# Optimization experiments

Hardware: AMD Instinct MI355X
Metric: run time of the kernel (lower is better)

The kernel has to match this reference:

```python
import jax, jax.numpy as jnp
from jax import lax
import numpy as np

D_MODEL, N_STATES, N_GROUPS, K_CONV = 1024, 16, 8, 4
BATCH, LENGTH = 2, 2048


def setup_inputs() -> dict:
    key = jax.random.key(0)
    ks = jax.random.split(key, 8)
    x = jax.random.normal(ks[0], (BATCH, LENGTH, D_MODEL), dtype=jnp.float32)
    in_proj_w = jax.random.normal(ks[1], (2 * D_MODEL, D_MODEL), dtype=jnp.float32) * 0.02
    in_proj_b = jnp.zeros((2 * D_MODEL,), dtype=jnp.float32)
    delta_proj_w = jax.random.uniform(ks[2], (D_MODEL, D_MODEL), dtype=jnp.float32, minval=0.001, maxval=0.1)
    a_log = jnp.log(jnp.tile(jnp.arange(1, N_STATES + 1, dtype=jnp.float32), (D_MODEL, 1)))
    b_proj_w = jax.random.normal(ks[3], (N_GROUPS * N_STATES, D_MODEL), dtype=jnp.float32) * 1e-4
    b_proj_b = jnp.zeros((N_GROUPS * N_STATES,), dtype=jnp.float32)
    c_param = jax.random.normal(ks[4], (D_MODEL, N_STATES), dtype=jnp.float32) * 0.02
    # depthwise conv (groups = d_model): kernel [D, 1, K]
    conv_w = jax.random.normal(ks[5], (D_MODEL, 1, K_CONV), dtype=jnp.float32) * (1.0 / np.sqrt(K_CONV))
    conv_b = jnp.zeros((D_MODEL,), dtype=jnp.float32)
    return {"x": x, "in_proj_w": in_proj_w, "in_proj_b": in_proj_b,
            "delta_proj_w": delta_proj_w, "a_log": a_log,
            "b_proj_w": b_proj_w, "b_proj_b": b_proj_b, "c_param": c_param,
            "conv_w": conv_w, "conv_b": conv_b}


def _causal_conv(u, conv_w, conv_b):
    # u: [B, L, D] -> depthwise causal conv along L
    D = u.shape[-1]
    K = conv_w.shape[-1]
    uc = jnp.transpose(u, (0, 2, 1))  # [B, D, L]
    uc = lax.conv_general_dilated(uc, conv_w, window_strides=(1,),
                                  padding=[(K - 1, 0)], feature_group_count=D,
                                  dimension_numbers=("NCH", "OIH", "NCH"))
    uc = uc + conv_b[None, :, None]
    return jnp.transpose(uc, (0, 2, 1))  # [B, L, D]


def _selective_scan(delta, A, Bmat, c_param, u):
    # delta,u: [B,L,D]; A: [D,N]; Bmat: [B,L,G,N]; c_param: [D,N]
    Bsz, L, D = delta.shape
    N = A.shape[1]
    G = Bmat.shape[2]
    Bexp = jnp.repeat(Bmat, D // G, axis=2)            # [B,L,D,N]
    dA = jnp.exp(delta[..., None] * A)                  # [B,L,D,N]
    dBu = (delta * u)[..., None] * Bexp                 # [B,L,D,N]

    def step(h, xs):
        da, dbu = xs
        h = da * h + dbu                                # [B,D,N]
        y = jnp.einsum("bdn,dn->bd", h, c_param)
        return h, y

    h0 = jnp.zeros((Bsz, D, N), dtype=delta.dtype)
    _, ys = lax.scan(step, h0, (jnp.moveaxis(dA, 1, 0), jnp.moveaxis(dBu, 1, 0)))
    return jnp.moveaxis(ys, 0, 1)                       # [B,L,D]


def reference(x, in_proj_w, in_proj_b, delta_proj_w, a_log, b_proj_w, b_proj_b, c_param, conv_w, conv_b):
    Bsz, L, _ = x.shape
    N = a_log.shape[1]
    G = b_proj_w.shape[0] // N
    xp = x @ in_proj_w.T + in_proj_b                    # [B,L,2D]
    u, v = jnp.split(xp, 2, axis=-1)
    delta = jax.nn.softplus(u @ delta_proj_w.T)         # [B,L,D]
    A = -jnp.exp(a_log)                                 # [D,N]
    Bmat = (u @ b_proj_w.T + b_proj_b).reshape(Bsz, L, G, N)
    u_conv = jax.nn.silu(_causal_conv(u, conv_w, conv_b))
    y = _selective_scan(delta, A, Bmat, c_param, u_conv)
    return y * jax.nn.silu(v)
```

## Files before the change

### kernel.cpp

```cpp
#include <hip/hip_runtime.h>
#include <math.h>

#define LTOT 2048
#define MROWS 4096
#define CHK 64
#define NCH (LTOT / CHK)
#define SPAD 20

typedef short bf16x8 __attribute__((ext_vector_type(8)));
typedef float f32x4  __attribute__((ext_vector_type(4)));

__device__ __forceinline__ unsigned short bf16_rne(float f) {
  unsigned u = __float_as_uint(f);
  u += 0x7FFF + ((u >> 16) & 1);
  return (unsigned short)(u >> 16);
}
__device__ __forceinline__ float bf16_to_f(unsigned short h) {
  return __uint_as_float(((unsigned)h) << 16);
}
__device__ __forceinline__ float softplus_f(float x) {
  return (x > 15.f) ? x : log1pf(expf(x));
}
__device__ __forceinline__ float silu_f(float x) {
  return x / (1.f + expf(-x));
}

__global__ __launch_bounds__(256) void k_prep(
    const float* __restrict__ x, const float* __restrict__ w1,
    const float* __restrict__ dw, const float* __restrict__ bw,
    const float* __restrict__ b1, const float* __restrict__ bb,
    unsigned short* __restrict__ xh, unsigned short* __restrict__ wfh,
    unsigned short* __restrict__ wdbAh, unsigned short* __restrict__ wdbAl,
    unsigned short* __restrict__ w1th, unsigned short* __restrict__ w1tl,
    float* __restrict__ bfull) {
  __shared__ float ts[64][65];
  const int blk = blockIdx.x;
  const int t = threadIdx.x;

  if (blk < 6144) {
    const float* src; unsigned short* h; int i;
    if (blk < 4096) { src = x;  h = xh;  i = blk * 256 + t; }
    else            { src = w1; h = wfh; i = (blk - 4096) * 256 + t; }
    const float4 v = ((const float4*)src)[i];
    ushort4 hh;
    hh.x = bf16_rne(v.x); hh.y = bf16_rne(v.y);
    hh.z = bf16_rne(v.z); hh.w = bf16_rne(v.w);
    ((ushort4*)h)[i] = hh;
  } else if (blk < 7296) {
    const float* src; unsigned short *h, *l; int i;
    if (blk < 7168) { src = dw; h = wdbAh; l = wdbAl; i = (blk - 6144) * 256 + t; }
    else            { src = bw; h = wdbAh + (size_t)1024*1024; l = wdbAl + (size_t)1024*1024;
                      i = (blk - 7168) * 256 + t; }
    const float4 v = ((const float4*)src)[i];
    ushort4 hh, ll;
    hh.x = bf16_rne(v.x); ll.x = bf16_rne(v.x - bf16_to_f(hh.x));
    hh.y = bf16_rne(v.y); ll.y = bf16_rne(v.y - bf16_to_f(hh.y));
    hh.z = bf16_rne(v.z); ll.z = bf16_rne(v.z - bf16_to_f(hh.z));
    hh.w = bf16_rne(v.w); ll.w = bf16_rne(v.w - bf16_to_f(hh.w));
    ((ushort4*)h)[i] = hh;
    ((ushort4*)l)[i] = ll;
  } else if (blk < 7552) {
    const int s = blk - 7296;
    const int k0 = (s & 15) * 64, j0 = (s >> 4) * 64;
    const int r = t >> 4, c4 = (t & 15) * 4;
    #pragma unroll
    for (int p = 0; p < 4; ++p) {
      const int row = p * 16 + r;
      const float4 v = *(const float4*)&w1[(size_t)(j0 + row) * 1024 + k0 + c4];
      ts[row][c4] = v.x; ts[row][c4+1] = v.y; ts[row][c4+2] = v.z; ts[row][c4+3] = v.w;
    }
    __syncthreads();
    #pragma unroll
    for (int p = 0; p < 4; ++p) {
      const int rk = p * 16 + r;
      ushort4 hh, ll;
      float f;
      f = ts[c4+0][rk]; hh.x = bf16_rne(f); ll.x = bf16_rne(f - bf16_to_f(hh.x));
      f = ts[c4+1][rk]; hh.y = bf16_rne(f); ll.y = bf16_rne(f - bf16_to_f(hh.y));
      f = ts[c4+2][rk]; hh.z = bf16_rne(f); ll.z = bf16_rne(f - bf16_to_f(hh.z));
      f = ts[c4+3][rk]; hh.w = bf16_rne(f); ll.w = bf16_rne(f - bf16_to_f(hh.w));
      *(ushort4*)&w1th[(size_t)(k0 + rk) * 1024 + j0 + c4] = hh;
      *(ushort4*)&w1tl[(size_t)(k0 + rk) * 1024 + j0 + c4] = ll;
    }
  } else {
    const int j = (blk - 7552) * 16 + (t >> 4);
    const int lane16 = t & 15;
    const float* W = (j < 1024) ? (dw + (size_t)j * 1024) : (bw + (size_t)(j - 1024) * 1024);
    float s = 0.f;
    for (int i = 0; i < 64; ++i) {
      const int k = lane16 + i * 16;
      s = fmaf(b1[k], W[k], s);
    }
    s += __shfl_xor(s, 8, 16);
    s += __shfl_xor(s, 4, 16);
    s += __shfl_xor(s, 2, 16);
    s += __shfl_xor(s, 1, 16);
    if (lane16 == 0) bfull[j] = s + ((j >= 1024) ? bb[j - 1024] : 0.f);
  }
}

__global__ __launch_bounds__(256) void k_wcomp3(
    const unsigned short* __restrict__ Ah_g, const unsigned short* __restrict__ Al_g,
    const unsigned short* __restrict__ Bh_g, const unsigned short* __restrict__ Bl_g,
    float* __restrict__ part) {
  __shared__ __align__(16) unsigned short LAh[128*32];
  __shared__ __align__(16) unsigned short LAl[128*32];
  __shared__ __align__(16) unsigned short LBh[128*32];
  __shared__ __align__(16) unsigned short LBl[128*32];
  const int t = threadIdx.x;
  const int wave = t >> 6, lane = t & 63;
  const int m0 = blockIdx.y * 128;
  const int n0 = blockIdx.x * 128;
  const int kb = blockIdx.z * 256;
  const int wr = wave >> 1, wc = wave & 1;
  const int ln = lane & 15, kq = lane >> 4;
  const int srow = lane >> 2, scol = (lane & 3) * 8;

  f32x4 acc[4][4];
  #pragma unroll
  for (int i = 0; i < 4; ++i)
    #pragma unroll
    for (int j = 0; j < 4; ++j) acc[i][j] = (f32x4){0.f, 0.f, 0.f, 0.f};

  const unsigned short* pAh = Ah_g + (size_t)m0 * 1024;
  const unsigned short* pAl = Al_g + (size_t)m0 * 1024;
  const unsigned short* pBh = Bh_g + (size_t)n0 * 1024;
  const unsigned short* pBl = Bl_g + (size_t)n0 * 1024;

  auto stage = [&](const unsigned short* g, unsigned short* lds, int k0) {
    #pragma unroll
    for (int r = 0; r < 2; ++r) {
      const unsigned short* gp = g + (size_t)(r * 64 + wave * 16 + srow) * 1024 + k0 + scol;
      unsigned short* lp = lds + (r * 64 + wave * 16) * 32;
      __builtin_amdgcn_global_load_lds((const __attribute__((address_space(1))) void*)gp,
                                       (__attribute__((address_space(3))) void*)lp, 16, 0, 0);
    }
  };

  for (int k0 = kb; k0 < kb + 256; k0 += 32) {
    __syncthreads();
    stage(pAh, LAh, k0);
    stage(pAl, LAl, k0);
    stage(pBh, LBh, k0);
    stage(pBl, LBl, k0);
    __syncthreads();
    bf16x8 ah[4], al[4], bh[4], bl[4];
    #pragma unroll
    for (int i = 0; i < 4; ++i) {
      const int ar = (wr * 64 + i * 16 + ln) * 32 + kq * 8;
      const int br = (wc * 64 + i * 16 + ln) * 32 + kq * 8;
      ah[i] = *(const bf16x8*)&LAh[ar];
      al[i] = *(const bf16x8*)&LAl[ar];
      bh[i] = *(const bf16x8*)&LBh[br];
      bl[i] = *(const bf16x8*)&LBl[br];
    }
    #pragma unroll
    for (int i = 0; i < 4; ++i)
      #pragma unroll
      for (int j = 0; j < 4; ++j) {
        acc[i][j] = __builtin_amdgcn_mfma_f32_16x16x32_bf16(ah[i], bh[j], acc[i][j], 0, 0, 0);
        acc[i][j] = __builtin_amdgcn_mfma_f32_16x16x32_bf16(ah[i], bl[j], acc[i][j], 0, 0, 0);
        acc[i][j] = __builtin_amdgcn_mfma_f32_16x16x32_bf16(al[i], bh[j], acc[i][j], 0, 0, 0);
      }
  }

  float* pout = part + (size_t)blockIdx.z * 1152 * 1024;
  #pragma unroll
  for (int nj = 0; nj < 4; ++nj) {
    const int kcol = n0 + wc * 64 + nj * 16 + ln;
    #pragma unroll
    for (int mi = 0; mi < 4; ++mi) {
      const int i = m0 + wr * 64 + mi * 16 + kq * 4;
      #pragma unroll
      for (int j = 0; j < 4; ++j)
        pout[(size_t)(i + j) * 1024 + kcol] = acc[mi][nj][j];
    }
  }
}

__global__ void k_wred(const float* __restrict__ part, unsigned short* __restrict__ outh) {
  const int e = blockIdx.x * 256 + threadIdx.x;
  const int i = e >> 8;
  const int k4 = (e & 255) * 4;
  const size_t stride = (size_t)1152 * 1024;
  const size_t off = (size_t)i * 1024 + k4;
  float4 s = *(const float4*)&part[off];
  #pragma unroll
  for (int p = 1; p < 4; ++p) {
    const float4 q = *(const float4*)&part[p * stride + off];
    s.x += q.x; s.y += q.y; s.z += q.z; s.w += q.w;
  }
  const int rbase = (i < 1024) ? (2176 + i) : (1024 + i);
  ushort4 hh;
  hh.x = bf16_rne(s.x); hh.y = bf16_rne(s.y); hh.z = bf16_rne(s.z); hh.w = bf16_rne(s.w);
  *(ushort4*)&outh[(size_t)rbase * 1024 + k4] = hh;
}

__global__ __launch_bounds__(256) void k_mm_u(
    const unsigned short* __restrict__ xh, const unsigned short* __restrict__ wfh,
    const float* __restrict__ b1, const float* __restrict__ bfull,
    float* __restrict__ u_, float* __restrict__ v_,
    float* __restrict__ delta, float* __restrict__ Bm) {
  __shared__ __align__(16) unsigned short LA[2][128*64];
  __shared__ __align__(16) unsigned short LB[2][128*64];
  const int t = threadIdx.x;
  const int wave = t >> 6, lane = t & 63;
  const int flat = blockIdx.x;
  const int wg = (flat & 7) * 100 + (flat >> 3);
  const int tn = wg % 25;
  const int m0 = (wg / 25) * 128;
  const int wr = wave >> 1, wc = wave & 1;
  const int ln = lane & 15, kq = lane >> 4;
  const int srow = lane >> 3;
  const int scb  = ((lane & 7) ^ (lane >> 3)) * 8;

  f32x4 acc[4][4];
  #pragma unroll
  for (int i = 0; i < 4; ++i)
    #pragma unroll
    for (int j = 0; j < 4; ++j) acc[i][j] = (f32x4){0.f, 0.f, 0.f, 0.f};

  const unsigned short* pAh = xh + (size_t)m0 * 1024;
  const unsigned short* pBh = wfh + (size_t)(tn * 128) * 1024;

  auto stage = [&](const unsigned short* g, unsigned short* lds, int k0) {
    #pragma unroll
    for (int r = 0; r < 4; ++r) {
      const int rowb = wave * 32 + r * 8;
      const unsigned short* gp = g + (size_t)(rowb + srow) * 1024 + k0 + scb;
      unsigned short* lp = lds + rowb * 64;
      __builtin_amdgcn_global_load_lds((const __attribute__((address_space(1))) void*)gp,
                                       (__attribute__((address_space(3))) void*)lp, 16, 0, 0);
    }
  };

  stage(pAh, LA[0], 0);
  stage(pBh, LB[0], 0);

  for (int tt = 0; tt < 16; ++tt) {
    const int cur = tt & 1;
    if (tt < 15) {
      stage(pAh, LA[cur ^ 1], (tt + 1) * 64);
      stage(pBh, LB[cur ^ 1], (tt + 1) * 64);
      asm volatile("s_waitcnt vmcnt(8)" ::: "memory");
    } else {
      asm volatile("s_waitcnt vmcnt(0)" ::: "memory");
    }
    __builtin_amdgcn_s_barrier();
    __builtin_amdgcn_sched_barrier(0);

    const unsigned short* la = LA[cur];
    const unsigned short* lb = LB[cur];
    #pragma unroll
    for (int kh = 0; kh < 2; ++kh) {
      bf16x8 ah[4], bh[4];
      #pragma unroll
      for (int i = 0; i < 4; ++i) {
        const int arow = wr * 64 + i * 16 + ln;
        const int brow = wc * 64 + i * 16 + ln;
        const int ablk = ((kh * 4 + kq) ^ (arow & 7)) * 8;
        const int bblk = ((kh * 4 + kq) ^ (brow & 7)) * 8;
        ah[i] = *(const bf16x8*)&la[arow * 64 + ablk];
        bh[i] = *(const bf16x8*)&lb[brow * 64 + bblk];
      }
      #pragma unroll
      for (int i = 0; i < 4; ++i)
        #pragma unroll
        for (int j = 0; j < 4; ++j)
          acc[i][j] = __builtin_amdgcn_mfma_f32_16x16x32_bf16(ah[i], bh[j], acc[i][j], 0, 0, 0);
    }

    if (tt < 15) {
      __builtin_amdgcn_sched_barrier(0);
      __builtin_amdgcn_s_barrier();
    }
  }

  #pragma unroll
  for (int nj = 0; nj < 4; ++nj) {
    const int colg = tn * 128 + wc * 64 + nj * 16 + ln;
    float bv;
    if (colg < 2048)      bv = b1[colg];
    else if (colg < 2176) bv = bfull[1024 + colg - 2048];
    else                  bv = bfull[colg - 2176];
    #pragma unroll
    for (int mi = 0; mi < 4; ++mi) {
      const int row = m0 + wr * 64 + mi * 16 + kq * 4;
      #pragma unroll
      for (int j = 0; j < 4; ++j) {
        const float val = acc[mi][nj][j] + bv;
        if (tn < 8)        u_[(size_t)(row + j) * 1024 + colg] = val;
        else if (tn < 16)  v_[(size_t)(row + j) * 1024 + colg - 1024] = val;
        else if (tn == 16) Bm[(size_t)(row + j) * 128 + colg - 2048] = val;
        else               delta[(size_t)(row + j) * 1024 + colg - 2176] = softplus_f(val);
      }
    }
  }
}

__global__ __launch_bounds__(256) void k_scanA(
    const float* __restrict__ delta, const float* __restrict__ u_,
    const float* __restrict__ Bm, const float* __restrict__ a_log,
    const float* __restrict__ cw, const float* __restrict__ cb,
    float* __restrict__ hend, float* __restrict__ Pp)
{
  __shared__ float sru[68][SPAD];
  __shared__ float sd[CHK][SPAD];
  __shared__ float sb[CHK][SPAD];
  __shared__ float suc[CHK][SPAD];
  const int t = threadIdx.x;
  const int bid = blockIdx.x;
  const int dblk = bid & 63;
  const int ch   = (bid >> 6) & (NCH - 1);
  const int b    = bid >> 11;
  const int d0 = dblk * 16;
  const int g  = dblk >> 3;
  const int l0 = ch * CHK;
  const size_t mb = (size_t)b * LTOT;

  {
    const int lrow = t >> 2;
    const int lc4  = (t & 3) * 4;
    const size_t r = mb + l0 + lrow;
    float4 rd = *(const float4*)&delta[r*1024 + d0 + lc4];
    float4 rb = *(const float4*)&Bm[r*128 + g*16 + lc4];
    *(float4*)&sd[lrow][lc4] = rd;
    *(float4*)&sb[lrow][lc4] = rb;
    const int sl = l0 + lrow - 4;
    float4 ru = (sl >= 0) ? *(const float4*)&u_[(mb + sl)*1024 + d0 + lc4]
                          : (float4){0.f, 0.f, 0.f, 0.f};
    *(float4*)&sru[lrow][lc4] = ru;
    if (t < 16) {
      const int rr2 = 64 + (t >> 2);
      const int sl2 = l0 + rr2 - 4;
      float4 r2 = *(const float4*)&u_[(mb + sl2)*1024 + d0 + (t & 3) * 4];
      *(float4*)&sru[rr2][(t & 3) * 4] = r2;
    }
  }
  __syncthreads();
  {
    const int c = t & 15;
    const int rb4 = (t >> 4) * 4;
    const float4 cwf = *(const float4*)&cw[(d0 + c) * 4];
    const float cbf = cb[d0 + c];
    #pragma unroll
    for (int q = 0; q < 4; ++q) {
      const int l = rb4 + q;
      float a = cbf;
      a = fmaf(sru[l+1][c], cwf.x, a);
      a = fmaf(sru[l+2][c], cwf.y, a);
      a = fmaf(sru[l+3][c], cwf.z, a);
      a = fmaf(sru[l+4][c], cwf.w, a);
      suc[l][c] = silu_f(a);
    }
  }
  __syncthreads();

  const int gi = t >> 4;
  const int n  = t & 15;
  const int d  = d0 + gi;
  const float A2 = -expf(a_log[d*16 + n]) * 1.4426950408889634f;

  float h = 0.f, P = 1.f;
  #pragma unroll 8
  for (int l = 0; l < CHK; ++l) {
    const float dv = sd[l][gi];
    const float uv = suc[l][gi];
    const float bv = sb[l][n];
    const float da = exp2f(dv * A2);
    P *= da;
    h = fmaf(da, h, dv * uv * bv);
  }
  const size_t idx = ((size_t)(b*NCH + ch) * 1024 + d) * 16 + n;
  hend[idx] = h;
  Pp[idx]   = P;
}

__global__ void k_scanB(float* hP, const float* __restrict__ Pp)
{
  const int t = blockIdx.x * 256 + threadIdx.x;
  const int b  = t >> 14;
  const int dn = t & 16383;
  float H = 0.f;
  for (int ch = 0; ch < NCH; ++ch) {
    const size_t idx = ((size_t)(b*NCH + ch) << 14) + dn;
    const float he = hP[idx];
    const float P  = Pp[idx];
    hP[idx] = H;
    H = fmaf(P, H, he);
  }
}

__global__ __launch_bounds__(256) void k_scanC(
    const float* __restrict__ v_, const float* __restrict__ delta,
    const float* __restrict__ u_, const float* __restrict__ Bm,
    const float* __restrict__ a_log, const float* __restrict__ cp,
    const float* __restrict__ cw, const float* __restrict__ cb,
    const float* __restrict__ Hstart, float* __restrict__ out)
{
  __shared__ float sru[68][SPAD];
  __shared__ float sd[CHK][SPAD];
  __shared__ float sb[CHK][SPAD];
  __shared__ float suc[CHK][SPAD];
  __shared__ float sv[CHK][SPAD];
  __shared__ float sy[CHK][SPAD];
  const int t = threadIdx.x;
  const int bid = blockIdx.x;
  const int dblk = bid & 63;
  const int ch   = (bid >> 6) & (NCH - 1);
  const int b    = bid >> 11;
  const int d0 = dblk * 16;
  const int g  = dblk >> 3;
  const int l0 = ch * CHK;
  const size_t mb = (size_t)b * LTOT;

  {
    const int lrow = t >> 2;
    const int lc4  = (t & 3) * 4;
    const size_t r = mb + l0 + lrow;
    float4 rd = *(const float4*)&delta[r*1024 + d0 + lc4];
    float4 rb = *(const float4*)&Bm[r*128 + g*16 + lc4];
    float4 rv = *(const float4*)&v_[r*1024 + d0 + lc4];
    *(float4*)&sd[lrow][lc4] = rd;
    *(float4*)&sb[lrow][lc4] = rb;
    *(float4*)&sv[lrow][lc4] = rv;
    const int sl = l0 + lrow - 4;
    float4 ru = (sl >= 0) ? *(const float4*)&u_[(mb + sl)*1024 + d0 + lc4]
                          : (float4){0.f, 0.f, 0.f, 0.f};
    *(float4*)&sru[lrow][lc4] = ru;
    if (t < 16) {
      const int rr2 = 64 + (t >> 2);
      const int sl2 = l0 + rr2 - 4;
      float4 r2 = *(const float4*)&u_[(mb + sl2)*1024 + d0 + (t & 3) * 4];
      *(float4*)&sru[rr2][(t & 3) * 4] = r2;
    }
  }
  __syncthreads();
  {
    const int c = t & 15;
    const int rb4 = (t >> 4) * 4;
    const float4 cwf = *(const float4*)&cw[(d0 + c) * 4];
    const float cbf = cb[d0 + c];
    #pragma unroll
    for (int q = 0; q < 4; ++q) {
      const int l = rb4 + q;
      float a = cbf;
      a = fmaf(sru[l+1][c], cwf.x, a);
      a = fmaf(sru[l+2][c], cwf.y, a);
      a = fmaf(sru[l+3][c], cwf.z, a);
      a = fmaf(sru[l+4][c], cwf.w, a);
      suc[l][c] = silu_f(a);
    }
  }
  __syncthreads();

  const int gi = t >> 4;
  const int n  = t & 15;
  const int d  = d0 + gi;
  const float A2 = -expf(a_log[d*16 + n]) * 1.4426950408889634f;
  const float cc = cp[d*16 + n];
  float h = Hstart[((size_t)(b*NCH + ch) * 1024 + d) * 16 + n];

  #pragma unroll
  for (int l16 = 0; l16 < CHK; l16 += 16) {
    float p[16];
    #pragma unroll
    for (int j = 0; j < 16; ++j) {
      const int l = l16 + j;
      const float dv = sd[l][gi];
      const float uv = suc[l][gi];
      const float bv = sb[l][n];
      const float da = exp2f(dv * A2);
      h = fmaf(da, h, dv * uv * bv);
      p[j] = h * cc;
    }
    float q8[8];
    #pragma unroll
    for (int j = 0; j < 8; ++j) {
      const float send = (n & 8) ? p[j]     : p[j + 8];
      const float keep = (n & 8) ? p[j + 8] : p[j];
      q8[j] = keep + __shfl_xor(send, 8, 16);
    }
    float q4[4];
    #pragma unroll
    for (int j = 0; j < 4; ++j) {
      const float send = (n & 4) ? q8[j]     : q8[j + 4];
      const float keep = (n & 4) ? q8[j + 4] : q8[j];
      q4[j] = keep + __shfl_xor(send, 4, 16);
    }
    float q2[2];
    #pragma unroll
    for (int j = 0; j < 2; ++j) {
      const float send = (n & 2) ? q4[j]     : q4[j + 2];
      const float keep = (n & 2) ? q4[j + 2] : q4[j];
      q2[j] = keep + __shfl_xor(send, 2, 16);
    }
    {
      const float send = (n & 1) ? q2[0] : q2[1];
      const float keep = (n & 1) ? q2[1] : q2[0];
      sy[l16 + n][gi] = keep + __shfl_xor(send, 1, 16);
    }
  }

  __syncthreads();
  const int rr = t >> 4;
  const int c  = t & 15;
  #pragma unroll
  for (int k = 0; k < 4; ++k) {
    const int r = rr + k * 16;
    const float vv = sv[r][c];
    out[(mb + l0 + r) * 1024 + d0 + c] = sy[r][c] * silu_f(vv);
  }
}

extern "C" void kernel_launch(void* const* d_in, const int* in_sizes, int n_in,
                              void* d_out, int out_size, void* d_ws, size_t ws_size,
                              hipStream_t stream) {
  const float* x    = (const float*)d_in[0];
  const float* w1   = (const float*)d_in[1];
  const float* b1   = (const float*)d_in[2];
  const float* dw   = (const float*)d_in[3];
  const float* alog = (const float*)d_in[4];
  const float* bw   = (const float*)d_in[5];
  const float* bb   = (const float*)d_in[6];
  const float* cp   = (const float*)d_in[7];
  const float* cw   = (const float*)d_in[8];
  const float* cb   = (const float*)d_in[9];
  float* out = (float*)d_out;

  const size_t M4 = (size_t)MROWS * 1024;
  float* u_    = (float*)d_ws;
  float* v_    = u_ + M4;
  float* delta = v_ + M4;
  float* Bm    = delta + M4;
  unsigned short* xh  = (unsigned short*)(Bm + (size_t)MROWS * 128);
  unsigned short* xl  = xh + M4;
  unsigned short* wfh = xl + M4;
  unsigned short* wfl = wfh + (size_t)3200 * 1024;
  float* bfull = (float*)(wfl + (size_t)3200 * 1024);
  float* wpart = (float*)d_ws;
  unsigned short* wdbAh = (unsigned short*)delta;
  unsigned short* wdbAl = wdbAh + (size_t)1152 * 1024;
  unsigned short* w1th  = wdbAl + (size_t)1152 * 1024;
  unsigned short* w1tl  = w1th + (size_t)1024 * 1024;
  float* hend = (float*)wfh;
  float* Pp   = hend + (size_t)2 * NCH * 1024 * 16;

  k_prep<<<7624, 256, 0, stream>>>(x, w1, dw, bw, b1, bb,
                                   xh, wfh, wdbAh, wdbAl, w1th, w1tl, bfull);
  k_wcomp3<<<dim3(8, 9, 4), 256, 0, stream>>>(wdbAh, wdbAl, w1th, w1tl, wpart);
  k_wred<<<1152, 256, 0, stream>>>(wpart, wfh);
  k_mm_u<<<800, 256, 0, stream>>>(xh, wfh, b1, bfull, u_, v_, delta, Bm);
  k_scanA<<<2 * NCH * 64, 256, 0, stream>>>(delta, u_, Bm, alog, cw, cb, hend, Pp);
  k_scanB<<<128, 256, 0, stream>>>(hend, Pp);
  k_scanC<<<2 * NCH * 64, 256, 0, stream>>>(v_, delta, u_, Bm, alog, cp, cw, cb, hend, out);
}
```

Before: 186.5 us.

## Stage weight tiles through registers with two-deep prefetch in k_mm_u GEMM

The GEMM's weight (B) tile is no longer loaded with direct global-to-LDS loads. Each thread now holds it in a pair of register buffers, prefetched two k-steps ahead, and writes it to LDS with a swizzle before the barrier. Activation tiles still use direct LDS loads. The aim is deeper latency hiding for the weight stream and freeing the vmcnt budget. The cost is higher register pressure and extra LDS write and wait instructions inside the main loop.

Measured after the change: 187.4 us. Within noise of the previous version (+0.5%).

```diff
diff --git a/kernel.cpp b/kernel.cpp
--- a/kernel.cpp
+++ b/kernel.cpp
@@ -9,6 +9,7 @@
 
 typedef short bf16x8 __attribute__((ext_vector_type(8)));
 typedef float f32x4  __attribute__((ext_vector_type(4)));
+typedef unsigned int u32x4 __attribute__((ext_vector_type(4)));
 
 __device__ __forceinline__ unsigned short bf16_rne(float f) {
   unsigned u = __float_as_uint(f);
@@ -202,7 +203,7 @@
     float* __restrict__ u_, float* __restrict__ v_,
     float* __restrict__ delta, float* __restrict__ Bm) {
   __shared__ __align__(16) unsigned short LA[2][128*64];
-  __shared__ __align__(16) unsigned short LB[2][128*64];
+  __shared__ __align__(16) unsigned short LW[2][128*64];
   const int t = threadIdx.x;
   const int wave = t >> 6, lane = t & 63;
   const int flat = blockIdx.x;
@@ -214,6 +215,15 @@
   const int srow = lane >> 3;
   const int scb  = ((lane & 7) ^ (lane >> 3)) * 8;
 
+  int wdst[4]; size_t wsrc[4];
+  #pragma unroll
+  for (int q = 0; q < 4; ++q) {
+    const int row = q * 32 + (t >> 3);
+    const int blk = t & 7;
+    wdst[q] = row * 64 + ((blk ^ (row & 7)) * 8);
+    wsrc[q] = (size_t)row * 1024 + blk * 8;
+  }
+
   f32x4 acc[4][4];
   #pragma unroll
   for (int i = 0; i < 4; ++i)
@@ -221,36 +231,52 @@
     for (int j = 0; j < 4; ++j) acc[i][j] = (f32x4){0.f, 0.f, 0.f, 0.f};
 
   const unsigned short* pAh = xh + (size_t)m0 * 1024;
-  const unsigned short* pBh = wfh + (size_t)(tn * 128) * 1024;
-
-  auto stage = [&](const unsigned short* g, unsigned short* lds, int k0) {
+  const unsigned short* pW  = wfh + (size_t)(tn * 128) * 1024;
+
+  auto stageA = [&](unsigned short* lds, int k0) {
     #pragma unroll
     for (int r = 0; r < 4; ++r) {
       const int rowb = wave * 32 + r * 8;
-      const unsigned short* gp = g + (size_t)(rowb + srow) * 1024 + k0 + scb;
+      const unsigned short* gp = pAh + (size_t)(rowb + srow) * 1024 + k0 + scb;
       unsigned short* lp = lds + rowb * 64;
       __builtin_amdgcn_global_load_lds((const __attribute__((address_space(1))) void*)gp,
                                        (__attribute__((address_space(3))) void*)lp, 16, 0, 0);
     }
   };
 
-  stage(pAh, LA[0], 0);
-  stage(pBh, LB[0], 0);
-
-  for (int tt = 0; tt < 16; ++tt) {
-    const int cur = tt & 1;
-    if (tt < 15) {
-      stage(pAh, LA[cur ^ 1], (tt + 1) * 64);
-      stage(pBh, LB[cur ^ 1], (tt + 1) * 64);
-      asm volatile("s_waitcnt vmcnt(8)" ::: "memory");
-    } else {
-      asm volatile("s_waitcnt vmcnt(0)" ::: "memory");
-    }
+  u32x4 wreg[2][4];
+
+  #pragma unroll
+  for (int q = 0; q < 4; ++q) wreg[0][q] = *(const u32x4*)&pW[wsrc[q]];
+  __builtin_amdgcn_sched_barrier(0);
+  stageA(LA[0], 0);
+  __builtin_amdgcn_sched_barrier(0);
+  #pragma unroll
+  for (int q = 0; q < 4; ++q) wreg[1][q] = *(const u32x4*)&pW[wsrc[q] + 64];
+  __builtin_amdgcn_sched_barrier(0);
+
+  #pragma unroll
+  for (int s = 0; s < 16; ++s) {
+    const int cur = s & 1;
+    if (s == 15) asm volatile("s_waitcnt vmcnt(0)" ::: "memory");
+    else         asm volatile("s_waitcnt vmcnt(4)" ::: "memory");
+    #pragma unroll
+    for (int q = 0; q < 4; ++q) *(u32x4*)&LW[cur][wdst[q]] = wreg[cur][q];
+    asm volatile("s_waitcnt lgkmcnt(0)" ::: "memory");
+    __builtin_amdgcn_sched_barrier(0);
+    if (s < 15) stageA(LA[cur ^ 1], (s + 1) * 64);
+    __builtin_amdgcn_sched_barrier(0);
+    if (s < 14) {
+      #pragma unroll
+      for (int q = 0; q < 4; ++q)
+        wreg[cur][q] = *(const u32x4*)&pW[wsrc[q] + (size_t)(s + 2) * 64];
+    }
+    __builtin_amdgcn_sched_barrier(0);
     __builtin_amdgcn_s_barrier();
     __builtin_amdgcn_sched_barrier(0);
 
     const unsigned short* la = LA[cur];
-    const unsigned short* lb = LB[cur];
+    const unsigned short* lw = LW[cur];
     #pragma unroll
     for (int kh = 0; kh < 2; ++kh) {
       bf16x8 ah[4], bh[4];
@@ -261,7 +287,7 @@
         const int ablk = ((kh * 4 + kq) ^ (arow & 7)) * 8;
         const int bblk = ((kh * 4 + kq) ^ (brow & 7)) * 8;
         ah[i] = *(const bf16x8*)&la[arow * 64 + ablk];
-        bh[i] = *(const bf16x8*)&lb[brow * 64 + bblk];
+        bh[i] = *(const bf16x8*)&lw[brow * 64 + bblk];
       }
       #pragma unroll
       for (int i = 0; i < 4; ++i)
@@ -270,7 +296,7 @@
           acc[i][j] = __builtin_amdgcn_mfma_f32_16x16x32_bf16(ah[i], bh[j], acc[i][j], 0, 0, 0);
     }
 
-    if (tt < 15) {
+    if (s < 15) {
       __builtin_amdgcn_sched_barrier(0);
       __builtin_amdgcn_s_barrier();
     }
```
